# Kernel tuning notes

Hardware: AMD Instinct MI355X
Metric: run time of the kernel (lower is better)

## Reference

```python
import jax, jax.numpy as jnp
import numpy as np

CAPSULES = 64
CAPSULE_DIM = 32
ROUTINGS = 3
EPS = 1e-7  # K.epsilon()


def setup_inputs() -> dict:
    key = jax.random.key(0)
    k1, k2 = jax.random.split(key)
    inputs = jax.random.normal(k1, (32, 2048, 16), dtype=jnp.float32)
    # W: (capsules, input_capsules, capsule_dim, input_capsule_dim), glorot-ish scale
    W = jax.random.normal(k2, (CAPSULES, 2048, CAPSULE_DIM, 16), dtype=jnp.float32) * 0.05
    return {"inputs": inputs, "W": W}


def squash(s):
    # s: [..., capsule_dim]
    s_norm = jnp.sum(jnp.square(s), axis=-1, keepdims=True)
    scale = s_norm / (1.0 + s_norm) / jnp.sqrt(s_norm + EPS)
    return s * scale


def reference(inputs, W):
    # inputs: [b, i, j] (batch, input_capsules, input_capsule_dim)
    # W:      [c, i, d, j] (capsules, input_capsules, capsule_dim, input_capsule_dim)
    # u_hat = batched predictions: [b, c, i, d]
    u_hat = jnp.einsum('bij,cidj->bcid', inputs, W)
    B = inputs.shape[0]
    b = jnp.zeros((B, CAPSULES, u_hat.shape[2]), dtype=u_hat.dtype)
    v = None
    for r in range(ROUTINGS):
        c = jax.nn.softmax(b, axis=1)              # softmax over capsules axis
        s = jnp.einsum('bci,bcid->bcd', c, u_hat)  # weighted sum over input capsules
        v = squash(s)                              # [b, c, d]
        # Original updates b for r > 0; the update at the final iteration has no
        # effect on the output, so it is skipped for efficiency (identical math).
        if 0 < r < ROUTINGS - 1:
            b = b + jnp.einsum('bcd,bcid->bci', v, u_hat)
    return v
```

## Files before the change

### kernel.cpp

```cpp
#include <hip/hip_runtime.h>
#include <math.h>

#define B_   32
#define I_   2048
#define J_   16
#define C_   64
#define D_   32
#define CD_  2048
#define W_CSTR (I_*D_*J_)
#define W_ISTR (D_*J_)
#define X_BSTR (I_*J_)
#define EPS_ 1e-7f

typedef _Float16 half8 __attribute__((ext_vector_type(8)));
typedef float    f32x16 __attribute__((ext_vector_type(16)));


__device__ __forceinline__ half8 wfrag_from_f32(const float* __restrict__ W,
                                                int c, int i, int l) {
  const float* wp = W + (size_t)c*W_CSTR + (size_t)i*W_ISTR
                      + (size_t)(l & 31)*J_ + ((l >> 5) << 3);
  float4 a = *(const float4*)wp;
  float4 b = *(const float4*)(wp + 4);
  half8 h;
  h[0]=(_Float16)a.x; h[1]=(_Float16)a.y; h[2]=(_Float16)a.z; h[3]=(_Float16)a.w;
  h[4]=(_Float16)b.x; h[5]=(_Float16)b.y; h[6]=(_Float16)b.z; h[7]=(_Float16)b.w;
  return h;
}

__global__ __launch_bounds__(256) void k_xpack(const float* __restrict__ x,
                                               half8* __restrict__ xh) {
  const int tg = blockIdx.x*256 + threadIdx.x;
  const int i = tg >> 6, l = tg & 63;
  const int b = l & 31, jb = (l >> 5) << 3;
  const float* xp = x + (size_t)b*X_BSTR + (size_t)i*J_ + jb;
  float4 a = *(const float4*)xp;
  float4 bb = *(const float4*)(xp + 4);
  half8 h;
  h[0]=(_Float16)a.x;  h[1]=(_Float16)a.y;  h[2]=(_Float16)a.z;  h[3]=(_Float16)a.w;
  h[4]=(_Float16)bb.x; h[5]=(_Float16)bb.y; h[6]=(_Float16)bb.z; h[7]=(_Float16)bb.w;
  xh[tg] = h;
}

template<bool WRITE_WB>
__global__ __launch_bounds__(512, 4) void k_passA(const float* __restrict__ W,
                                                  const half8* __restrict__ xh,
                                                  float* __restrict__ part,
                                                  _Float16* __restrict__ WB) {
  const int t = threadIdx.x, l = t & 63, w = t >> 6;
  const int ic = blockIdx.x, c = blockIdx.y*8 + w;
  f32x16 acc = {};
  #pragma unroll 4
  for (int ii = 0; ii < 32; ii++) {
    const int i = ic*32 + ii;
    half8 wf = wfrag_from_f32(W, c, i, l);
    half8 xf = xh[(size_t)i*64 + l];
    if (WRITE_WB)
      *(half8*)(WB + ((size_t)c*I_ + i)*512 + (size_t)l*8) = wf;
    acc = __builtin_amdgcn_mfma_f32_32x32x16_f16(xf, wf, acc, 0, 0, 0);
  }
  const int col = c*32 + (l & 31), h4 = (l >> 5)*4;
  #pragma unroll
  for (int r = 0; r < 16; r++) {
    const int row = (r & 3) + 8*(r >> 2) + h4;
    part[(size_t)ic*(B_*CD_) + (size_t)row*CD_ + col] = acc[r];
  }
}

__global__ __launch_bounds__(256) void k_redsquash(const float* __restrict__ part,
                                                   float* __restrict__ outp,
                                                   float scale) {
  const int g = blockIdx.x*256 + threadIdx.x;
  float s = 0.f;
  #pragma unroll 8
  for (int ch = 0; ch < 64; ch++) s += part[(size_t)ch*(B_*CD_) + g];
  s *= scale;
  float sn = s*s;
  #pragma unroll
  for (int off = 1; off <= 16; off <<= 1) sn += __shfl_xor(sn, off);
  const float sc = sn / ((1.f + sn) * sqrtf(sn + EPS_));
  outp[g] = s*sc;
}

template<bool USE_WB>
__global__ __launch_bounds__(512, 4) void k_blogit(const float* __restrict__ W,
                                                   const _Float16* __restrict__ WB,
                                                   const half8* __restrict__ xh,
                                                   const float* __restrict__ v1,
                                                   float* __restrict__ b1) {
  const int t = threadIdx.x, l = t & 63, w = t >> 6;
  const int ic = blockIdx.x, c = blockIdx.y*8 + w;
  const int d = l & 31, h4 = (l >> 5)*4;

  float v1r[16];
  #pragma unroll
  for (int r = 0; r < 16; r++) {
    const int row = (r & 3) + 8*(r >> 2) + h4;
    v1r[r] = v1[((size_t)row*64 + c)*32 + d];
  }
  const int orow = (((l >> 4) & 1) ? 8 : 0) + (((l >> 3) & 1) ? 4 : 0)
                 + (((l >> 2) & 1) ? 2 : 0) + ((l >> 1) & 1);
  const int wrow = (orow & 3) + 8*(orow >> 2) + h4;

  const bool s4 = (l & 16), s3 = (l & 8), s2b = (l & 4), s1 = (l & 2);

  #pragma unroll 2
  for (int ii = 0; ii < 32; ii++) {
    const int i = ic*32 + ii;
    half8 wf = USE_WB ? *(const half8*)(WB + ((size_t)c*I_ + i)*512 + (size_t)l*8)
                      : wfrag_from_f32(W, c, i, l);
    half8 xf = xh[(size_t)i*64 + l];
    f32x16 z = {};
    f32x16 u = __builtin_amdgcn_mfma_f32_32x32x16_f16(xf, wf, z, 0, 0, 0);

    float p[16];
    #pragma unroll
    for (int r = 0; r < 16; r++) p[r] = v1r[r] * u[r];
    #pragma unroll
    for (int r = 0; r < 16; r++) p[r] += __shfl_xor(p[r], 16);
    float q[8];
    #pragma unroll
    for (int r = 0; r < 8; r++) q[r] = s4 ? p[r+8] : p[r];
    #pragma unroll
    for (int r = 0; r < 8; r++) q[r] += __shfl_xor(q[r], 8);
    float q4[4];
    #pragma unroll
    for (int r = 0; r < 4; r++) q4[r] = s3 ? q[r+4] : q[r];
    #pragma unroll
    for (int r = 0; r < 4; r++) q4[r] += __shfl_xor(q4[r], 4);
    float q2[2];
    #pragma unroll
    for (int r = 0; r < 2; r++) q2[r] = s2b ? q4[r+2] : q4[r];
    #pragma unroll
    for (int r = 0; r < 2; r++) q2[r] += __shfl_xor(q2[r], 2);
    float y = s1 ? q2[1] : q2[0];
    y += __shfl_xor(y, 1);

    if ((l & 1) == 0)
      b1[((size_t)i*64 + c)*32 + wrow] = y;
  }
}

__global__ __launch_bounds__(256) void k_softmaxT(const float* __restrict__ b1,
                                                  float* __restrict__ c2) {
  __shared__ float ST[2048];
  __shared__ float PM[256], PS[256];
  const int i = blockIdx.x, t = threadIdx.x;
  const float* src = b1 + (size_t)i*2048;
  *(float4*)(ST + t*8)     = *(const float4*)(src + t*8);
  *(float4*)(ST + t*8 + 4) = *(const float4*)(src + t*8 + 4);
  __syncthreads();
  const int b = t & 31, ck = t >> 5;
  float m = -1e30f;
  #pragma unroll
  for (int cc = 0; cc < 8; cc++) m = fmaxf(m, ST[(ck*8 + cc)*32 + b]);
  PM[t] = m;
  __syncthreads();
  #pragma unroll
  for (int k = 0; k < 8; k++) m = fmaxf(m, PM[k*32 + b]);
  float s = 0.f;
  #pragma unroll
  for (int cc = 0; cc < 8; cc++) {
    const int idx = (ck*8 + cc)*32 + b;
    const float e = __expf(ST[idx] - m);
    s += e;
    ST[idx] = e;
  }
  PS[t] = s;
  __syncthreads();
  s = 0.f;
  #pragma unroll
  for (int k = 0; k < 8; k++) s += PS[k*32 + b];
  const float inv = 1.f / s;
  float* dst = c2 + (size_t)i*2048;
  #pragma unroll
  for (int cc = 0; cc < 8; cc++) {
    const int idx = (ck*8 + cc)*32 + b;
    dst[idx] = ST[idx] * inv;
  }
}

template<bool USE_WB>
__global__ __launch_bounds__(512, 4) void k_passB2(const float* __restrict__ W,
                                                   const _Float16* __restrict__ WB,
                                                   const half8* __restrict__ xh,
                                                   const float* __restrict__ c2,
                                                   float* __restrict__ part) {
  const int t = threadIdx.x, l = t & 63, w = t >> 6;
  const int ic = blockIdx.x, c = blockIdx.y*8 + w;
  const int h4 = (l >> 5)*4;
  f32x16 s2 = {};
  #pragma unroll 2
  for (int ii = 0; ii < 32; ii++) {
    const int i = ic*32 + ii;
    half8 wf = USE_WB ? *(const half8*)(WB + ((size_t)c*I_ + i)*512 + (size_t)l*8)
                      : wfrag_from_f32(W, c, i, l);
    half8 xf = xh[(size_t)i*64 + l];
    f32x16 z = {};
    f32x16 u = __builtin_amdgcn_mfma_f32_32x32x16_f16(xf, wf, z, 0, 0, 0);
    const float* cp = c2 + ((size_t)i*64 + c)*32 + h4;
    float4 c0 = *(const float4*)(cp);
    float4 c1 = *(const float4*)(cp + 8);
    float4 cB = *(const float4*)(cp + 16);
    float4 c3 = *(const float4*)(cp + 24);
    s2[0] += c0.x*u[0];  s2[1] += c0.y*u[1];  s2[2]  += c0.z*u[2];  s2[3]  += c0.w*u[3];
    s2[4] += c1.x*u[4];  s2[5] += c1.y*u[5];  s2[6]  += c1.z*u[6];  s2[7]  += c1.w*u[7];
    s2[8] += cB.x*u[8];  s2[9] += cB.y*u[9];  s2[10] += cB.z*u[10]; s2[11] += cB.w*u[11];
    s2[12]+= c3.x*u[12]; s2[13]+= c3.y*u[13]; s2[14] += c3.z*u[14]; s2[15] += c3.w*u[15];
  }
  const int col = c*32 + (l & 31);
  #pragma unroll
  for (int r = 0; r < 16; r++) {
    const int row = (r & 3) + 8*(r >> 2) + h4;
    part[(size_t)ic*(B_*CD_) + (size_t)row*CD_ + col] = s2[r];
  }
}

extern "C" void kernel_launch(void* const* d_in, const int* in_sizes, int n_in,
                              void* d_out, int out_size, void* d_ws, size_t ws_size,
                              hipStream_t stream) {
  (void)in_sizes; (void)n_in; (void)out_size;
  const float* x = (const float*)d_in[0];
  const float* W = (const float*)d_in[1];
  float* out = (float*)d_out;

  const size_t MiB = 1024*1024;
  char* ws = (char*)d_ws;
  const bool big = ws_size >= 163*MiB;

  _Float16* WB; float *part, *b1, *c2, *xhp, *v1;
  if (big) {
    WB    = (_Float16*)(ws);
    part  = (float*)(ws + 128*MiB);
    b1    = part;
    c2    = (float*)(ws + 144*MiB);
    xhp   = (float*)(ws + 160*MiB);
    v1    = (float*)(ws + 162*MiB);
  } else {
    WB    = nullptr;
    part  = (float*)(ws);
    b1    = part;
    c2    = (float*)(ws + 16*MiB);
    xhp   = (float*)(ws + 32*MiB);
    v1    = (float*)(ws + 34*MiB);
  }
  half8* xh = (half8*)xhp;

  k_xpack<<<512, 256, 0, stream>>>(x, xh);
  if (big) k_passA<true ><<<dim3(64, 8), 512, 0, stream>>>(W, xh, part, WB);
  else     k_passA<false><<<dim3(64, 8), 512, 0, stream>>>(W, xh, part, WB);
  k_redsquash<<<256, 256, 0, stream>>>(part, v1, 1.f/64.f);
  if (big) k_blogit<true ><<<dim3(64, 8), 512, 0, stream>>>(W, WB, xh, v1, b1);
  else     k_blogit<false><<<dim3(64, 8), 512, 0, stream>>>(W, WB, xh, v1, b1);
  k_softmaxT<<<2048, 256, 0, stream>>>(b1, c2);
  if (big) k_passB2<true ><<<dim3(64, 8), 512, 0, stream>>>(W, WB, xh, c2, part);
  else     k_passB2<false><<<dim3(64, 8), 512, 0, stream>>>(W, WB, xh, c2, part);
  k_redsquash<<<256, 256, 0, stream>>>(part, out, 1.f);
}
```

Baseline: 540.8 us.

## Transpose MFMA operand order so batch lands on lanes, simplifying logit reductions

Swaps the MFMA A/B operands so each lane holds one batch element and the accumulator registers span the capsule dimension. The partial-sum buffer and v1 are re-laid out as [c][d][b] to match. The b-logit kernel's multi-stage shuffle/select reduction becomes a register-local dot product plus one cross-half shuffle, and passB2 loads one coupling scalar per lane instead of four float4s. The reduce/squash kernel now uses 1024-thread blocks with a shared-memory tree over d, and writes a transposed final output. This trades extra syncthreads in a small kernel for less shuffle and load work in the heavy kernels.

```diff
diff --git a/kernel.cpp b/kernel.cpp
--- a/kernel.cpp
+++ b/kernel.cpp
@@ -49,6 +49,7 @@
                                                   _Float16* __restrict__ WB) {
   const int t = threadIdx.x, l = t & 63, w = t >> 6;
   const int ic = blockIdx.x, c = blockIdx.y*8 + w;
+  const int b = l & 31, h4 = (l >> 5)*4;
   f32x16 acc = {};
   #pragma unroll 4
   for (int ii = 0; ii < 32; ii++) {
@@ -57,29 +58,38 @@
     half8 xf = xh[(size_t)i*64 + l];
     if (WRITE_WB)
       *(half8*)(WB + ((size_t)c*I_ + i)*512 + (size_t)l*8) = wf;
-    acc = __builtin_amdgcn_mfma_f32_32x32x16_f16(xf, wf, acc, 0, 0, 0);
-  }
-  const int col = c*32 + (l & 31), h4 = (l >> 5)*4;
+    acc = __builtin_amdgcn_mfma_f32_32x32x16_f16(wf, xf, acc, 0, 0, 0);
+  }
   #pragma unroll
   for (int r = 0; r < 16; r++) {
-    const int row = (r & 3) + 8*(r >> 2) + h4;
-    part[(size_t)ic*(B_*CD_) + (size_t)row*CD_ + col] = acc[r];
-  }
-}
-
-__global__ __launch_bounds__(256) void k_redsquash(const float* __restrict__ part,
-                                                   float* __restrict__ outp,
-                                                   float scale) {
-  const int g = blockIdx.x*256 + threadIdx.x;
+    const int dr = (r & 3) + 8*(r >> 2) + h4;
+    part[(size_t)ic*(B_*CD_) + ((size_t)c*32 + dr)*32 + b] = acc[r];
+  }
+}
+
+template<bool TOUT>
+__global__ __launch_bounds__(1024) void k_redsquash(const float* __restrict__ part,
+                                                    float* __restrict__ outp,
+                                                    float scale) {
+  __shared__ float SN[1024];
+  const int c = blockIdx.x, t = threadIdx.x;
+  const int d = t >> 5, b = t & 31;
   float s = 0.f;
   #pragma unroll 8
-  for (int ch = 0; ch < 64; ch++) s += part[(size_t)ch*(B_*CD_) + g];
+  for (int ch = 0; ch < 64; ch++) s += part[(size_t)ch*(B_*CD_) + c*1024 + t];
   s *= scale;
-  float sn = s*s;
-  #pragma unroll
-  for (int off = 1; off <= 16; off <<= 1) sn += __shfl_xor(sn, off);
+  SN[t] = s*s;
+  __syncthreads();
+  #pragma unroll
+  for (int st = 16; st >= 1; st >>= 1) {
+    if (d < st) SN[t] += SN[t + st*32];
+    __syncthreads();
+  }
+  const float sn = SN[b];
   const float sc = sn / ((1.f + sn) * sqrtf(sn + EPS_));
-  outp[g] = s*sc;
+  const float val = s*sc;
+  if (TOUT) outp[(size_t)b*CD_ + c*32 + d] = val;
+  else      outp[(size_t)c*1024 + t] = val;
 }
 
 template<bool USE_WB>
@@ -90,54 +100,29 @@
                                                    float* __restrict__ b1) {
   const int t = threadIdx.x, l = t & 63, w = t >> 6;
   const int ic = blockIdx.x, c = blockIdx.y*8 + w;
-  const int d = l & 31, h4 = (l >> 5)*4;
+  const int b = l & 31, h4 = (l >> 5)*4;
 
   float v1r[16];
   #pragma unroll
   for (int r = 0; r < 16; r++) {
-    const int row = (r & 3) + 8*(r >> 2) + h4;
-    v1r[r] = v1[((size_t)row*64 + c)*32 + d];
-  }
-  const int orow = (((l >> 4) & 1) ? 8 : 0) + (((l >> 3) & 1) ? 4 : 0)
-                 + (((l >> 2) & 1) ? 2 : 0) + ((l >> 1) & 1);
-  const int wrow = (orow & 3) + 8*(orow >> 2) + h4;
-
-  const bool s4 = (l & 16), s3 = (l & 8), s2b = (l & 4), s1 = (l & 2);
-
-  #pragma unroll 2
+    const int dr = (r & 3) + 8*(r >> 2) + h4;
+    v1r[r] = v1[(size_t)c*1024 + dr*32 + b];
+  }
+
+  #pragma unroll 4
   for (int ii = 0; ii < 32; ii++) {
     const int i = ic*32 + ii;
     half8 wf = USE_WB ? *(const half8*)(WB + ((size_t)c*I_ + i)*512 + (size_t)l*8)
                       : wfrag_from_f32(W, c, i, l);
     half8 xf = xh[(size_t)i*64 + l];
     f32x16 z = {};
-    f32x16 u = __builtin_amdgcn_mfma_f32_32x32x16_f16(xf, wf, z, 0, 0, 0);
-
-    float p[16];
+    f32x16 u = __builtin_amdgcn_mfma_f32_32x32x16_f16(wf, xf, z, 0, 0, 0);
+    float y = 0.f;
     #pragma unroll
-    for (int r = 0; r < 16; r++) p[r] = v1r[r] * u[r];
-    #pragma unroll
-    for (int r = 0; r < 16; r++) p[r] += __shfl_xor(p[r], 16);
-    float q[8];
-    #pragma unroll
-    for (int r = 0; r < 8; r++) q[r] = s4 ? p[r+8] : p[r];
-    #pragma unroll
-    for (int r = 0; r < 8; r++) q[r] += __shfl_xor(q[r], 8);
-    float q4[4];
-    #pragma unroll
-    for (int r = 0; r < 4; r++) q4[r] = s3 ? q[r+4] : q[r];
-    #pragma unroll
-    for (int r = 0; r < 4; r++) q4[r] += __shfl_xor(q4[r], 4);
-    float q2[2];
-    #pragma unroll
-    for (int r = 0; r < 2; r++) q2[r] = s2b ? q4[r+2] : q4[r];
-    #pragma unroll
-    for (int r = 0; r < 2; r++) q2[r] += __shfl_xor(q2[r], 2);
-    float y = s1 ? q2[1] : q2[0];
-    y += __shfl_xor(y, 1);
-
-    if ((l & 1) == 0)
-      b1[((size_t)i*64 + c)*32 + wrow] = y;
+    for (int r = 0; r < 16; r++) y += u[r]*v1r[r];
+    y += __shfl_xor(y, 32);
+    if (l < 32)
+      b1[((size_t)i*64 + c)*32 + b] = y;
   }
 }
 
@@ -188,31 +173,24 @@
                                                    float* __restrict__ part) {
   const int t = threadIdx.x, l = t & 63, w = t >> 6;
   const int ic = blockIdx.x, c = blockIdx.y*8 + w;
-  const int h4 = (l >> 5)*4;
+  const int b = l & 31, h4 = (l >> 5)*4;
   f32x16 s2 = {};
-  #pragma unroll 2
+  #pragma unroll 4
   for (int ii = 0; ii < 32; ii++) {
     const int i = ic*32 + ii;
     half8 wf = USE_WB ? *(const half8*)(WB + ((size_t)c*I_ + i)*512 + (size_t)l*8)
                       : wfrag_from_f32(W, c, i, l);
     half8 xf = xh[(size_t)i*64 + l];
     f32x16 z = {};
-    f32x16 u = __builtin_amdgcn_mfma_f32_32x32x16_f16(xf, wf, z, 0, 0, 0);
-    const float* cp = c2 + ((size_t)i*64 + c)*32 + h4;
-    float4 c0 = *(const float4*)(cp);
-    float4 c1 = *(const float4*)(cp + 8);
-    float4 cB = *(const float4*)(cp + 16);
-    float4 c3 = *(const float4*)(cp + 24);
-    s2[0] += c0.x*u[0];  s2[1] += c0.y*u[1];  s2[2]  += c0.z*u[2];  s2[3]  += c0.w*u[3];
-    s2[4] += c1.x*u[4];  s2[5] += c1.y*u[5];  s2[6]  += c1.z*u[6];  s2[7]  += c1.w*u[7];
-    s2[8] += cB.x*u[8];  s2[9] += cB.y*u[9];  s2[10] += cB.z*u[10]; s2[11] += cB.w*u[11];
-    s2[12]+= c3.x*u[12]; s2[13]+= c3.y*u[13]; s2[14] += c3.z*u[14]; s2[15] += c3.w*u[15];
-  }
-  const int col = c*32 + (l & 31);
+    f32x16 u = __builtin_amdgcn_mfma_f32_32x32x16_f16(wf, xf, z, 0, 0, 0);
+    const float cv = c2[((size_t)i*64 + c)*32 + b];
+    #pragma unroll
+    for (int r = 0; r < 16; r++) s2[r] += cv*u[r];
+  }
   #pragma unroll
   for (int r = 0; r < 16; r++) {
-    const int row = (r & 3) + 8*(r >> 2) + h4;
-    part[(size_t)ic*(B_*CD_) + (size_t)row*CD_ + col] = s2[r];
+    const int dr = (r & 3) + 8*(r >> 2) + h4;
+    part[(size_t)ic*(B_*CD_) + ((size_t)c*32 + dr)*32 + b] = s2[r];
   }
 }
 
@@ -249,11 +227,11 @@
   k_xpack<<<512, 256, 0, stream>>>(x, xh);
   if (big) k_passA<true ><<<dim3(64, 8), 512, 0, stream>>>(W, xh, part, WB);
   else     k_passA<false><<<dim3(64, 8), 512, 0, stream>>>(W, xh, part, WB);
-  k_redsquash<<<256, 256, 0, stream>>>(part, v1, 1.f/64.f);
+  k_redsquash<false><<<64, 1024, 0, stream>>>(part, v1, 1.f/64.f);
   if (big) k_blogit<true ><<<dim3(64, 8), 512, 0, stream>>>(W, WB, xh, v1, b1);
   else     k_blogit<false><<<dim3(64, 8), 512, 0, stream>>>(W, WB, xh, v1, b1);
   k_softmaxT<<<2048, 256, 0, stream>>>(b1, c2);
   if (big) k_passB2<true ><<<dim3(64, 8), 512, 0, stream>>>(W, WB, xh, c2, part);
   else     k_passB2<false><<<dim3(64, 8), 512, 0, stream>>>(W, WB, xh, c2, part);
-  k_redsquash<<<256, 256, 0, stream>>>(part, out, 1.f);
-}
+  k_redsquash<true><<<64, 1024, 0, stream>>>(part, out, 1.f);
+}
```

Result: faster. 456.3 us (-15.6%).
